# Kernel tuning notes

Measured on AMD Instinct MI355X. Metric: run time of the kernel, lower is better.

## Reference

```python
import jax, jax.numpy as jnp
import numpy as np

K = 27        # 3^3 kernel offsets for kernel_size=3, dimension=3
M = 50000     # kernel-map pairs per offset
N = 100000    # active voxels
C = 64        # channels
EPS = 1e-5


def setup_inputs() -> dict:
    key = jax.random.key(0)
    ks = jax.random.split(key, 5)
    scale = 1.0 / np.sqrt(K * C)
    return {
        "features": jax.random.normal(ks[0], (N, C), jnp.float32),
        "W1": jax.random.normal(ks[1], (K, C, C), jnp.float32) * scale,
        "gamma1": jnp.ones((C,), jnp.float32),
        "beta1": jnp.zeros((C,), jnp.float32),
        "W2": jax.random.normal(ks[2], (K, C, C), jnp.float32) * scale,
        "gamma2": jnp.ones((C,), jnp.float32),
        "beta2": jnp.zeros((C,), jnp.float32),
        "in_maps": jax.random.randint(ks[3], (K, M), 0, N, dtype=jnp.int32),
        "out_maps": jax.random.randint(ks[4], (K, M), 0, N, dtype=jnp.int32),
        "n": N,
    }


def sparse_conv(f, W, in_maps, out_maps, n):
    # gather-GEMM-scatter, the MinkowskiConvolution compute pattern
    gathered = f[in_maps]                              # [K, M, Cin]
    msgs = jnp.einsum('kmc,kcd->kmd', gathered, W)     # [K, M, Cout]
    cout = W.shape[-1]
    out = jnp.zeros((n, cout), f.dtype)
    return out.at[out_maps.reshape(-1)].add(msgs.reshape(-1, cout))


def batch_norm(x, gamma, beta):
    # BatchNorm1d over the [N, C] sparse feature matrix (training-mode batch stats)
    mu = x.mean(axis=0)
    var = x.var(axis=0)
    return (x - mu) * jax.lax.rsqrt(var + EPS) * gamma + beta


def reference(features, W1, gamma1, beta1, W2, gamma2, beta2, in_maps, out_maps, n):
    out = sparse_conv(features, W1, in_maps, out_maps, n)
    out = jax.nn.relu(batch_norm(out, gamma1, beta1))
    out = sparse_conv(out, W2, in_maps, out_maps, n)
    out = batch_norm(out, gamma2, beta2)
    # stride=1 and in_channels==out_channels -> downsample is None
    return jax.nn.relu(out + features)
```

## Files before the change

### kernel.cpp

```cpp
#include <hip/hip_runtime.h>

typedef __attribute__((ext_vector_type(8))) short bf16x8;
typedef __attribute__((ext_vector_type(4))) float f32x4;

#define KK 27
#define MM 50000
#define NV 100000
#define CC 64
#define EPSV 1e-5f
#define PPB 400

__device__ inline void split2(float x, unsigned short& h, unsigned short& l) {
    const unsigned u  = __float_as_uint(x);
    const unsigned hb = u & 0xFFFF0000u;
    h = (unsigned short)(hb >> 16);
    const float r = x - __uint_as_float(hb);
    const unsigned v = __float_as_uint(r);
    l = (unsigned short)((v + 0x7FFFu + ((v >> 16) & 1u)) >> 16);
}

__device__ inline unsigned short rne_bf16(float x) {
    const unsigned u = __float_as_uint(x);
    return (unsigned short)((u + 0x7FFFu + ((u >> 16) & 1u)) >> 16);
}

__global__ __launch_bounds__(256)
void split_planes(const float* __restrict__ x, unsigned short* __restrict__ P) {
    const int i = blockIdx.x * 256 + threadIdx.x;
    const int r = i >> 5, c2 = (i & 31) * 2;
    const float2 v = *(const float2*)(x + (size_t)r * CC + c2);
    unsigned short h0, l0, h1, l1;
    split2(v.x, h0, l0);
    split2(v.y, h1, l1);
    *(unsigned int*)(P + (size_t)r * 128 + c2)      = (unsigned)h0 | ((unsigned)h1 << 16);
    *(unsigned int*)(P + (size_t)r * 128 + 64 + c2) = (unsigned)l0 | ((unsigned)l1 << 16);
}

__global__ __launch_bounds__(256)
void csr_hist(const int* __restrict__ outm, int* __restrict__ cnt) {
    const int e = blockIdx.x * 256 + threadIdx.x;
    if (e < KK * MM) atomicAdd(&cnt[outm[e]], 1);
}

__global__ __launch_bounds__(1024)
void scan1(const int* __restrict__ cnt, int* __restrict__ off, int* __restrict__ bsum) {
    __shared__ int tmp[1024];
    const int t = threadIdx.x;
    const int i = blockIdx.x * 1024 + t;
    const int v = (i < NV) ? cnt[i] : 0;
    tmp[t] = v;
    __syncthreads();
    for (int d = 1; d < 1024; d <<= 1) {
        const int add = (t >= d) ? tmp[t - d] : 0;
        __syncthreads();
        tmp[t] += add;
        __syncthreads();
    }
    if (i < NV) off[i] = tmp[t] - v;
    if (t == 1023) bsum[blockIdx.x] = tmp[1023];
}

__global__ __launch_bounds__(128)
void scan2(int* __restrict__ bsum, int nb) {
    __shared__ int tmp[128];
    const int t = threadIdx.x;
    const int v = (t < nb) ? bsum[t] : 0;
    tmp[t] = v;
    __syncthreads();
    for (int d = 1; d < 128; d <<= 1) {
        const int add = (t >= d) ? tmp[t - d] : 0;
        __syncthreads();
        tmp[t] += add;
        __syncthreads();
    }
    if (t < nb) bsum[t] = tmp[t] - v;
}

__global__ __launch_bounds__(256)
void scan3(int* __restrict__ off, const int* __restrict__ bsum) {
    const int i = blockIdx.x * 256 + threadIdx.x;
    if (i < NV) off[i] += bsum[i >> 10];
    if (i == 0) off[NV] = KK * MM;
}

__global__ __launch_bounds__(256)
void csr_fill(const int* __restrict__ outm, const int* __restrict__ off,
              int* __restrict__ cur, int* __restrict__ dst) {
    const int e = blockIdx.x * 256 + threadIdx.x;
    if (e >= KK * MM) return;
    const int row = outm[e];
    const int pos = atomicAdd(&cur[row], 1);
    dst[e] = off[row] + pos;
}

#define MF(a, b, c) c = __builtin_amdgcn_mfma_f32_16x16x32_bf16(a, b, c, 0, 0, 0)

__global__ __launch_bounds__(256, 3)
void conv_gemm(const unsigned short* __restrict__ P, const float* __restrict__ W,
               const int* __restrict__ inm_all, const int* __restrict__ dst,
               unsigned short* __restrict__ msgs) {
    const int k   = blockIdx.y;
    const int L   = threadIdx.x & 63;
    const int wv  = threadIdx.x >> 6;
    const int g   = L >> 4;
    const int c16 = L & 15;

    __shared__ float lds[4352];

    {
        const float4* Wg  = (const float4*)(W + (size_t)k * CC * CC);
        float4*       Wl4 = (float4*)lds;
#pragma unroll
        for (int i = 0; i < 4; ++i)
            Wl4[threadIdx.x + 256 * i] = Wg[threadIdx.x + 256 * i];
    }
    __syncthreads();

    bf16x8 Wh[2][4], Wlo[2][4];
#pragma unroll
    for (int s = 0; s < 2; ++s)
#pragma unroll
        for (int t = 0; t < 4; ++t)
#pragma unroll
            for (int j = 0; j < 8; ++j) {
                const float w = lds[(g * 8 + j + 32 * s) * CC + 16 * t + c16];
                unsigned short h, lo;
                split2(w, h, lo);
                Wh[s][t][j]  = (short)h;
                Wlo[s][t][j] = (short)lo;
            }
    __syncthreads();

    float* ldsC = lds + wv * 1088;

    const int* inm = inm_all + (size_t)k * MM;
    const int pstart = blockIdx.x * PPB;
    const int pend   = min(MM, pstart + PPB);

    int base = pstart + wv * 16;
    if (base + 16 > pend) return;

    const unsigned short* rp = P + (size_t)inm[base + c16] * 128;
    bf16x8 ah0 = *(const bf16x8*)(rp +      g * 8);
    bf16x8 ah1 = *(const bf16x8*)(rp + 32 + g * 8);
    bf16x8 al0 = *(const bf16x8*)(rp + 64 + g * 8);
    bf16x8 al1 = *(const bf16x8*)(rp + 96 + g * 8);

    while (true) {
        const int  nbase = base + 64;
        const bool hasn  = (nbase + 16 <= pend);
        bf16x8 nh0, nh1, nl0, nl1;
        if (hasn) {
            const unsigned short* np = P + (size_t)inm[nbase + c16] * 128;
            nh0 = *(const bf16x8*)(np +      g * 8);
            nh1 = *(const bf16x8*)(np + 32 + g * 8);
            nl0 = *(const bf16x8*)(np + 64 + g * 8);
            nl1 = *(const bf16x8*)(np + 96 + g * 8);
        }

        f32x4 acc0 = {0.f, 0.f, 0.f, 0.f}, acc1 = acc0, acc2 = acc0, acc3 = acc0;
        MF(ah0, Wh[0][0], acc0); MF(ah0, Wh[0][1], acc1); MF(ah0, Wh[0][2], acc2); MF(ah0, Wh[0][3], acc3);
        MF(ah1, Wh[1][0], acc0); MF(ah1, Wh[1][1], acc1); MF(ah1, Wh[1][2], acc2); MF(ah1, Wh[1][3], acc3);
        MF(al0, Wh[0][0], acc0); MF(al0, Wh[0][1], acc1); MF(al0, Wh[0][2], acc2); MF(al0, Wh[0][3], acc3);
        MF(al1, Wh[1][0], acc0); MF(al1, Wh[1][1], acc1); MF(al1, Wh[1][2], acc2); MF(al1, Wh[1][3], acc3);
        MF(ah0, Wlo[0][0], acc0); MF(ah0, Wlo[0][1], acc1); MF(ah0, Wlo[0][2], acc2); MF(ah0, Wlo[0][3], acc3);
        MF(ah1, Wlo[1][0], acc0); MF(ah1, Wlo[1][1], acc1); MF(ah1, Wlo[1][2], acc2); MF(ah1, Wlo[1][3], acc3);

#pragma unroll
        for (int j = 0; j < 4; ++j) {
            ldsC[(g * 4 + j) * 68 +      c16] = acc0[j];
            ldsC[(g * 4 + j) * 68 + 16 + c16] = acc1[j];
            ldsC[(g * 4 + j) * 68 + 32 + c16] = acc2[j];
            ldsC[(g * 4 + j) * 68 + 48 + c16] = acc3[j];
        }
        const int e0 = k * MM + base;
#pragma unroll
        for (int r = 0; r < 16; ++r) {
            const int d = dst[e0 + r];
            msgs[(size_t)d * CC + L] = rne_bf16(ldsC[r * 68 + L]);
        }

        if (!hasn) break;
        base = nbase;
        ah0 = nh0; ah1 = nh1; al0 = nl0; al1 = nl1;
    }
}

__global__ __launch_bounds__(256)
void csr_reduce_stats(const unsigned short* __restrict__ msgs,
                      const int* __restrict__ off,
                      float* __restrict__ out, float* __restrict__ stats) {
    const int L   = threadIdx.x & 63;
    const int wv  = threadIdx.x >> 6;
    const int q   = L & 15;
    const int sub = L >> 4;

    float sum0 = 0.f, sum1 = 0.f, sum2 = 0.f, sum3 = 0.f;
    float ssq0 = 0.f, ssq1 = 0.f, ssq2 = 0.f, ssq3 = 0.f;

    for (int n = blockIdx.x * 4 + wv; n < NV; n += gridDim.x * 4) {
        const int s = off[n], e = off[n + 1];
        float a0 = 0.f, a1 = 0.f, a2 = 0.f, a3 = 0.f;
        for (int i = s + sub; i < e; i += 4) {
            const uint2 v = *(const uint2*)(msgs + (size_t)i * CC + q * 4);
            a0 += __uint_as_float(v.x << 16);
            a1 += __uint_as_float(v.x & 0xFFFF0000u);
            a2 += __uint_as_float(v.y << 16);
            a3 += __uint_as_float(v.y & 0xFFFF0000u);
        }
        a0 += __shfl_xor(a0, 16); a1 += __shfl_xor(a1, 16);
        a2 += __shfl_xor(a2, 16); a3 += __shfl_xor(a3, 16);
        a0 += __shfl_xor(a0, 32); a1 += __shfl_xor(a1, 32);
        a2 += __shfl_xor(a2, 32); a3 += __shfl_xor(a3, 32);
        if (sub == 0) {
            const float4 r = {a0, a1, a2, a3};
            *(float4*)(out + (size_t)n * CC + q * 4) = r;
            sum0 += a0; ssq0 = fmaf(a0, a0, ssq0);
            sum1 += a1; ssq1 = fmaf(a1, a1, ssq1);
            sum2 += a2; ssq2 = fmaf(a2, a2, ssq2);
            sum3 += a3; ssq3 = fmaf(a3, a3, ssq3);
        }
    }

    __shared__ float red[2][4][CC];
    if (sub == 0) {
        red[0][wv][q * 4 + 0] = sum0; red[1][wv][q * 4 + 0] = ssq0;
        red[0][wv][q * 4 + 1] = sum1; red[1][wv][q * 4 + 1] = ssq1;
        red[0][wv][q * 4 + 2] = sum2; red[1][wv][q * 4 + 2] = ssq2;
        red[0][wv][q * 4 + 3] = sum3; red[1][wv][q * 4 + 3] = ssq3;
    }
    __syncthreads();
    if (threadIdx.x < CC) {
        const int c = threadIdx.x;
        const float ts  = red[0][0][c] + red[0][1][c] + red[0][2][c] + red[0][3][c];
        const float tss = red[1][0][c] + red[1][1][c] + red[1][2][c] + red[1][3][c];
        atomicAdd(&stats[c], ts);
        atomicAdd(&stats[CC + c], tss);
    }
}

__global__ __launch_bounds__(256)
void bn_relu_split(const float* __restrict__ x, const float* __restrict__ stats,
                   const float* __restrict__ gamma, const float* __restrict__ beta,
                   unsigned short* __restrict__ P) {
    const int i = blockIdx.x * 256 + threadIdx.x;
    const int r = i >> 5, c2 = (i & 31) * 2;
    float sc[2], sh[2];
#pragma unroll
    for (int j = 0; j < 2; ++j) {
        const int   c    = c2 + j;
        const float mu   = stats[c] * (1.f / NV);
        const float var  = fmaf(-mu, mu, stats[CC + c] * (1.f / NV));
        const float istd = rsqrtf(var + EPSV);
        sc[j] = gamma[c] * istd;
        sh[j] = fmaf(-mu, sc[j], beta[c]);
    }
    const float2 v = *(const float2*)(x + (size_t)r * CC + c2);
    const float y0 = fmaxf(fmaf(v.x, sc[0], sh[0]), 0.f);
    const float y1 = fmaxf(fmaf(v.y, sc[1], sh[1]), 0.f);
    unsigned short h0, l0, h1, l1;
    split2(y0, h0, l0);
    split2(y1, h1, l1);
    *(unsigned int*)(P + (size_t)r * 128 + c2)      = (unsigned)h0 | ((unsigned)h1 << 16);
    *(unsigned int*)(P + (size_t)r * 128 + 64 + c2) = (unsigned)l0 | ((unsigned)l1 << 16);
}

__global__ __launch_bounds__(256)
void bn_res_relu(float* __restrict__ x, const float* __restrict__ feat,
                 const float* __restrict__ stats,
                 const float* __restrict__ gamma, const float* __restrict__ beta) {
    const int tid   = blockIdx.x * blockDim.x + threadIdx.x;
    const int total = NV * CC / 4;
    const int cbase = (tid * 4) & (CC - 1);
    float scale[4], shift[4];
#pragma unroll
    for (int j = 0; j < 4; ++j) {
        const int   c    = cbase + j;
        const float mu   = stats[c] * (1.f / NV);
        const float var  = fmaf(-mu, mu, stats[CC + c] * (1.f / NV));
        const float istd = rsqrtf(var + EPSV);
        scale[j] = gamma[c] * istd;
        shift[j] = fmaf(-mu, scale[j], beta[c]);
    }
    float4*       x4 = (float4*)x;
    const float4* f4 = (const float4*)feat;
    for (int i = tid; i < total; i += gridDim.x * blockDim.x) {
        float4 v = x4[i];
        const float4 fr = f4[i];
        v.x = fmaxf(fmaf(v.x, scale[0], shift[0]) + fr.x, 0.f);
        v.y = fmaxf(fmaf(v.y, scale[1], shift[1]) + fr.y, 0.f);
        v.z = fmaxf(fmaf(v.z, scale[2], shift[2]) + fr.z, 0.f);
        v.w = fmaxf(fmaf(v.w, scale[3], shift[3]) + fr.w, 0.f);
        x4[i] = v;
    }
}

extern "C" void kernel_launch(void* const* d_in, const int* in_sizes, int n_in,
                              void* d_out, int out_size, void* d_ws, size_t ws_size,
                              hipStream_t stream) {
    const float* features = (const float*)d_in[0];
    const float* W1       = (const float*)d_in[1];
    const float* gamma1   = (const float*)d_in[2];
    const float* beta1    = (const float*)d_in[3];
    const float* W2       = (const float*)d_in[4];
    const float* gamma2   = (const float*)d_in[5];
    const float* beta2    = (const float*)d_in[6];
    const int*   in_maps  = (const int*)d_in[7];
    const int*   out_maps = (const int*)d_in[8];

    float* out = (float*)d_out;

    unsigned short* P     = (unsigned short*)d_ws;
    float*          stats = (float*)(P + (size_t)NV * 128);
    int*            cnt   = (int*)(stats + 256);
    int*            cur   = cnt + NV;
    int*            off   = cur + NV;
    int*            dst   = off + NV + 8;
    int*            bsum  = dst + KK * MM;
    unsigned short* msgs  = (unsigned short*)(bsum + 256);

    dim3 cgrid(MM / PPB, KK);

    hipMemsetAsync(stats, 0, (256 + 2 * NV) * sizeof(int), stream);

    split_planes<<<12500, 256, 0, stream>>>(features, P);

    csr_hist<<<(KK * MM + 255) / 256, 256, 0, stream>>>(out_maps, cnt);
    const int nb = (NV + 1023) / 1024;
    scan1<<<nb, 1024, 0, stream>>>(cnt, off, bsum);
    scan2<<<1, 128, 0, stream>>>(bsum, nb);
    scan3<<<(NV + 255) / 256, 256, 0, stream>>>(off, bsum);
    csr_fill<<<(KK * MM + 255) / 256, 256, 0, stream>>>(out_maps, off, cur, dst);

    conv_gemm<<<cgrid, 256, 0, stream>>>(P, W1, in_maps, dst, msgs);
    csr_reduce_stats<<<2048, 256, 0, stream>>>(msgs, off, out, stats);
    bn_relu_split<<<12500, 256, 0, stream>>>(out, stats, gamma1, beta1, P);

    conv_gemm<<<cgrid, 256, 0, stream>>>(P, W2, in_maps, dst, msgs);
    csr_reduce_stats<<<2048, 256, 0, stream>>>(msgs, off, out, stats + 128);
    bn_res_relu<<<1024, 256, 0, stream>>>(out, features, stats + 128, gamma2, beta2);
}
```

Before: 599.6 us.

## Merge CSR build and reduce/BN stages into cooperative grid-sync kernels

Replaces the six CSR-building and plane-split launches with one cooperative kernel that uses grid.sync between phases, and folds each BN/ReLU (or residual) pass into the reduction kernel after a grid-wide sync on the stats. The block scan now handles four elements per thread with 256 threads. conv_gemm's launch bounds are raised from 3 to 6 blocks per SM, which tightens the register budget. The aim is to cut launch gaps and tail effects. The cost is grid-sync overhead and a fixed 1024-block grid, where the reduction previously used 2048 blocks.

```diff
diff --git a/kernel.cpp b/kernel.cpp
--- a/kernel.cpp
+++ b/kernel.cpp
@@ -1,4 +1,7 @@
 #include <hip/hip_runtime.h>
+#include <hip/hip_cooperative_groups.h>
+
+namespace cg = cooperative_groups;
 
 typedef __attribute__((ext_vector_type(8))) short bf16x8;
 typedef __attribute__((ext_vector_type(4))) float f32x4;
@@ -25,77 +28,86 @@
 }
 
 __global__ __launch_bounds__(256)
-void split_planes(const float* __restrict__ x, unsigned short* __restrict__ P) {
-    const int i = blockIdx.x * 256 + threadIdx.x;
-    const int r = i >> 5, c2 = (i & 31) * 2;
-    const float2 v = *(const float2*)(x + (size_t)r * CC + c2);
-    unsigned short h0, l0, h1, l1;
-    split2(v.x, h0, l0);
-    split2(v.y, h1, l1);
-    *(unsigned int*)(P + (size_t)r * 128 + c2)      = (unsigned)h0 | ((unsigned)h1 << 16);
-    *(unsigned int*)(P + (size_t)r * 128 + 64 + c2) = (unsigned)l0 | ((unsigned)l1 << 16);
-}
-
-__global__ __launch_bounds__(256)
-void csr_hist(const int* __restrict__ outm, int* __restrict__ cnt) {
-    const int e = blockIdx.x * 256 + threadIdx.x;
-    if (e < KK * MM) atomicAdd(&cnt[outm[e]], 1);
-}
-
-__global__ __launch_bounds__(1024)
-void scan1(const int* __restrict__ cnt, int* __restrict__ off, int* __restrict__ bsum) {
-    __shared__ int tmp[1024];
-    const int t = threadIdx.x;
-    const int i = blockIdx.x * 1024 + t;
-    const int v = (i < NV) ? cnt[i] : 0;
-    tmp[t] = v;
-    __syncthreads();
-    for (int d = 1; d < 1024; d <<= 1) {
-        const int add = (t >= d) ? tmp[t - d] : 0;
+void build_coop(const float* __restrict__ x, unsigned short* __restrict__ P,
+                const int* __restrict__ outm,
+                int* __restrict__ cnt, int* __restrict__ cur,
+                int* __restrict__ off, int* __restrict__ dst,
+                int* __restrict__ bsum) {
+    cg::grid_group grid = cg::this_grid();
+    const int tid = blockIdx.x * 256 + threadIdx.x;
+    const int nth = gridDim.x * 256;
+
+    for (int i = tid; i < NV * 32; i += nth) {
+        const int r = i >> 5, c2 = (i & 31) * 2;
+        const float2 v = *(const float2*)(x + (size_t)r * CC + c2);
+        unsigned short h0, l0, h1, l1;
+        split2(v.x, h0, l0);
+        split2(v.y, h1, l1);
+        *(unsigned int*)(P + (size_t)r * 128 + c2)      = (unsigned)h0 | ((unsigned)h1 << 16);
+        *(unsigned int*)(P + (size_t)r * 128 + 64 + c2) = (unsigned)l0 | ((unsigned)l1 << 16);
+    }
+    for (int e = tid; e < KK * MM; e += nth) atomicAdd(&cnt[outm[e]], 1);
+    grid.sync();
+
+    if (blockIdx.x < (NV + 1023) / 1024) {
+        const int t    = threadIdx.x;
+        const int base = blockIdx.x * 1024 + t * 4;
+        int v[4], ts = 0;
+#pragma unroll
+        for (int j = 0; j < 4; ++j) {
+            v[j] = (base + j < NV) ? cnt[base + j] : 0;
+            ts += v[j];
+        }
+        __shared__ int ps[256];
+        ps[t] = ts;
         __syncthreads();
-        tmp[t] += add;
+        for (int d = 1; d < 256; d <<= 1) {
+            const int a = (t >= d) ? ps[t - d] : 0;
+            __syncthreads();
+            ps[t] += a;
+            __syncthreads();
+        }
+        int run = ps[t] - ts;
+#pragma unroll
+        for (int j = 0; j < 4; ++j) {
+            if (base + j < NV) off[base + j] = run;
+            run += v[j];
+        }
+        if (t == 255) bsum[blockIdx.x] = ps[255];
+    }
+    grid.sync();
+
+    if (blockIdx.x == 0) {
+        const int nb = (NV + 1023) / 1024;
+        const int t  = threadIdx.x;
+        __shared__ int tmp[256];
+        const int v = (t < nb) ? bsum[t] : 0;
+        tmp[t] = v;
         __syncthreads();
-    }
-    if (i < NV) off[i] = tmp[t] - v;
-    if (t == 1023) bsum[blockIdx.x] = tmp[1023];
-}
-
-__global__ __launch_bounds__(128)
-void scan2(int* __restrict__ bsum, int nb) {
-    __shared__ int tmp[128];
-    const int t = threadIdx.x;
-    const int v = (t < nb) ? bsum[t] : 0;
-    tmp[t] = v;
-    __syncthreads();
-    for (int d = 1; d < 128; d <<= 1) {
-        const int add = (t >= d) ? tmp[t - d] : 0;
-        __syncthreads();
-        tmp[t] += add;
-        __syncthreads();
-    }
-    if (t < nb) bsum[t] = tmp[t] - v;
-}
-
-__global__ __launch_bounds__(256)
-void scan3(int* __restrict__ off, const int* __restrict__ bsum) {
-    const int i = blockIdx.x * 256 + threadIdx.x;
-    if (i < NV) off[i] += bsum[i >> 10];
-    if (i == 0) off[NV] = KK * MM;
-}
-
-__global__ __launch_bounds__(256)
-void csr_fill(const int* __restrict__ outm, const int* __restrict__ off,
-              int* __restrict__ cur, int* __restrict__ dst) {
-    const int e = blockIdx.x * 256 + threadIdx.x;
-    if (e >= KK * MM) return;
-    const int row = outm[e];
-    const int pos = atomicAdd(&cur[row], 1);
-    dst[e] = off[row] + pos;
+        for (int d = 1; d < 256; d <<= 1) {
+            const int a = (t >= d) ? tmp[t - d] : 0;
+            __syncthreads();
+            tmp[t] += a;
+            __syncthreads();
+        }
+        if (t < nb) bsum[t] = tmp[t] - v;
+    }
+    grid.sync();
+
+    for (int i = tid; i < NV; i += nth) off[i] += bsum[i >> 10];
+    if (tid == 0) off[NV] = KK * MM;
+    grid.sync();
+
+    for (int e = tid; e < KK * MM; e += nth) {
+        const int row = outm[e];
+        const int pos = atomicAdd(&cur[row], 1);
+        dst[e] = off[row] + pos;
+    }
 }
 
 #define MF(a, b, c) c = __builtin_amdgcn_mfma_f32_16x16x32_bf16(a, b, c, 0, 0, 0)
 
-__global__ __launch_bounds__(256, 3)
+__global__ __launch_bounds__(256, 6)
 void conv_gemm(const unsigned short* __restrict__ P, const float* __restrict__ W,
                const int* __restrict__ inm_all, const int* __restrict__ dst,
                unsigned short* __restrict__ msgs) {
@@ -186,10 +198,13 @@
     }
 }
 
+template <int RES>
 __global__ __launch_bounds__(256)
-void csr_reduce_stats(const unsigned short* __restrict__ msgs,
-                      const int* __restrict__ off,
-                      float* __restrict__ out, float* __restrict__ stats) {
+void reduce_coop(const unsigned short* __restrict__ msgs, const int* __restrict__ off,
+                 float* __restrict__ out, float* __restrict__ stats,
+                 const float* __restrict__ gamma, const float* __restrict__ beta,
+                 unsigned short* __restrict__ P, const float* __restrict__ feat) {
+    cg::grid_group grid = cg::this_grid();
     const int L   = threadIdx.x & 63;
     const int wv  = threadIdx.x >> 6;
     const int q   = L & 15;
@@ -232,66 +247,60 @@
     __syncthreads();
     if (threadIdx.x < CC) {
         const int c = threadIdx.x;
-        const float ts  = red[0][0][c] + red[0][1][c] + red[0][2][c] + red[0][3][c];
-        const float tss = red[1][0][c] + red[1][1][c] + red[1][2][c] + red[1][3][c];
-        atomicAdd(&stats[c], ts);
-        atomicAdd(&stats[CC + c], tss);
-    }
-}
-
-__global__ __launch_bounds__(256)
-void bn_relu_split(const float* __restrict__ x, const float* __restrict__ stats,
-                   const float* __restrict__ gamma, const float* __restrict__ beta,
-                   unsigned short* __restrict__ P) {
-    const int i = blockIdx.x * 256 + threadIdx.x;
-    const int r = i >> 5, c2 = (i & 31) * 2;
-    float sc[2], sh[2];
-#pragma unroll
-    for (int j = 0; j < 2; ++j) {
-        const int   c    = c2 + j;
-        const float mu   = stats[c] * (1.f / NV);
-        const float var  = fmaf(-mu, mu, stats[CC + c] * (1.f / NV));
-        const float istd = rsqrtf(var + EPSV);
-        sc[j] = gamma[c] * istd;
-        sh[j] = fmaf(-mu, sc[j], beta[c]);
-    }
-    const float2 v = *(const float2*)(x + (size_t)r * CC + c2);
-    const float y0 = fmaxf(fmaf(v.x, sc[0], sh[0]), 0.f);
-    const float y1 = fmaxf(fmaf(v.y, sc[1], sh[1]), 0.f);
-    unsigned short h0, l0, h1, l1;
-    split2(y0, h0, l0);
-    split2(y1, h1, l1);
-    *(unsigned int*)(P + (size_t)r * 128 + c2)      = (unsigned)h0 | ((unsigned)h1 << 16);
-    *(unsigned int*)(P + (size_t)r * 128 + 64 + c2) = (unsigned)l0 | ((unsigned)l1 << 16);
-}
-
-__global__ __launch_bounds__(256)
-void bn_res_relu(float* __restrict__ x, const float* __restrict__ feat,
-                 const float* __restrict__ stats,
-                 const float* __restrict__ gamma, const float* __restrict__ beta) {
-    const int tid   = blockIdx.x * blockDim.x + threadIdx.x;
-    const int total = NV * CC / 4;
-    const int cbase = (tid * 4) & (CC - 1);
-    float scale[4], shift[4];
-#pragma unroll
-    for (int j = 0; j < 4; ++j) {
-        const int   c    = cbase + j;
-        const float mu   = stats[c] * (1.f / NV);
-        const float var  = fmaf(-mu, mu, stats[CC + c] * (1.f / NV));
-        const float istd = rsqrtf(var + EPSV);
-        scale[j] = gamma[c] * istd;
-        shift[j] = fmaf(-mu, scale[j], beta[c]);
-    }
-    float4*       x4 = (float4*)x;
-    const float4* f4 = (const float4*)feat;
-    for (int i = tid; i < total; i += gridDim.x * blockDim.x) {
-        float4 v = x4[i];
-        const float4 fr = f4[i];
-        v.x = fmaxf(fmaf(v.x, scale[0], shift[0]) + fr.x, 0.f);
-        v.y = fmaxf(fmaf(v.y, scale[1], shift[1]) + fr.y, 0.f);
-        v.z = fmaxf(fmaf(v.z, scale[2], shift[2]) + fr.z, 0.f);
-        v.w = fmaxf(fmaf(v.w, scale[3], shift[3]) + fr.w, 0.f);
-        x4[i] = v;
+        atomicAdd(&stats[c],      red[0][0][c] + red[0][1][c] + red[0][2][c] + red[0][3][c]);
+        atomicAdd(&stats[CC + c], red[1][0][c] + red[1][1][c] + red[1][2][c] + red[1][3][c]);
+    }
+
+    grid.sync();
+
+    const int tid = blockIdx.x * 256 + threadIdx.x;
+    const int nth = gridDim.x * 256;
+    if (RES == 0) {
+        for (int i = tid; i < NV * 32; i += nth) {
+            const int r = i >> 5, c2 = (i & 31) * 2;
+            float sc[2], sh[2];
+#pragma unroll
+            for (int j = 0; j < 2; ++j) {
+                const int   c    = c2 + j;
+                const float mu   = stats[c] * (1.f / NV);
+                const float var  = fmaf(-mu, mu, stats[CC + c] * (1.f / NV));
+                const float istd = rsqrtf(var + EPSV);
+                sc[j] = gamma[c] * istd;
+                sh[j] = fmaf(-mu, sc[j], beta[c]);
+            }
+            const float2 v = *(const float2*)(out + (size_t)r * CC + c2);
+            const float y0 = fmaxf(fmaf(v.x, sc[0], sh[0]), 0.f);
+            const float y1 = fmaxf(fmaf(v.y, sc[1], sh[1]), 0.f);
+            unsigned short h0, l0, h1, l1;
+            split2(y0, h0, l0);
+            split2(y1, h1, l1);
+            *(unsigned int*)(P + (size_t)r * 128 + c2)      = (unsigned)h0 | ((unsigned)h1 << 16);
+            *(unsigned int*)(P + (size_t)r * 128 + 64 + c2) = (unsigned)l0 | ((unsigned)l1 << 16);
+        }
+    } else {
+        const int total = NV * CC / 4;
+        const int cbase = (tid * 4) & (CC - 1);
+        float scale[4], shift[4];
+#pragma unroll
+        for (int j = 0; j < 4; ++j) {
+            const int   c    = cbase + j;
+            const float mu   = stats[c] * (1.f / NV);
+            const float var  = fmaf(-mu, mu, stats[CC + c] * (1.f / NV));
+            const float istd = rsqrtf(var + EPSV);
+            scale[j] = gamma[c] * istd;
+            shift[j] = fmaf(-mu, scale[j], beta[c]);
+        }
+        float4*       x4 = (float4*)out;
+        const float4* f4 = (const float4*)feat;
+        for (int i = tid; i < total; i += nth) {
+            float4 v = x4[i];
+            const float4 fr = f4[i];
+            v.x = fmaxf(fmaf(v.x, scale[0], shift[0]) + fr.x, 0.f);
+            v.y = fmaxf(fmaf(v.y, scale[1], shift[1]) + fr.y, 0.f);
+            v.z = fmaxf(fmaf(v.z, scale[2], shift[2]) + fr.z, 0.f);
+            v.w = fmaxf(fmaf(v.w, scale[3], shift[3]) + fr.w, 0.f);
+            x4[i] = v;
+        }
     }
 }
 
@@ -323,20 +332,31 @@
 
     hipMemsetAsync(stats, 0, (256 + 2 * NV) * sizeof(int), stream);
 
-    split_planes<<<12500, 256, 0, stream>>>(features, P);
-
-    csr_hist<<<(KK * MM + 255) / 256, 256, 0, stream>>>(out_maps, cnt);
-    const int nb = (NV + 1023) / 1024;
-    scan1<<<nb, 1024, 0, stream>>>(cnt, off, bsum);
-    scan2<<<1, 128, 0, stream>>>(bsum, nb);
-    scan3<<<(NV + 255) / 256, 256, 0, stream>>>(off, bsum);
-    csr_fill<<<(KK * MM + 255) / 256, 256, 0, stream>>>(out_maps, off, cur, dst);
+    {
+        void* args[] = {(void*)&features, (void*)&P, (void*)&out_maps,
+                        (void*)&cnt, (void*)&cur, (void*)&off, (void*)&dst,
+                        (void*)&bsum};
+        hipLaunchCooperativeKernel((void*)build_coop, dim3(1024), dim3(256),
+                                   args, 0, stream);
+    }
 
     conv_gemm<<<cgrid, 256, 0, stream>>>(P, W1, in_maps, dst, msgs);
-    csr_reduce_stats<<<2048, 256, 0, stream>>>(msgs, off, out, stats);
-    bn_relu_split<<<12500, 256, 0, stream>>>(out, stats, gamma1, beta1, P);
+
+    {
+        float* st = stats;
+        void* args[] = {(void*)&msgs, (void*)&off, (void*)&out, (void*)&st,
+                        (void*)&gamma1, (void*)&beta1, (void*)&P, (void*)&features};
+        hipLaunchCooperativeKernel((void*)reduce_coop<0>, dim3(1024), dim3(256),
+                                   args, 0, stream);
+    }
 
     conv_gemm<<<cgrid, 256, 0, stream>>>(P, W2, in_maps, dst, msgs);
-    csr_reduce_stats<<<2048, 256, 0, stream>>>(msgs, off, out, stats + 128);
-    bn_res_relu<<<1024, 256, 0, stream>>>(out, features, stats + 128, gamma2, beta2);
-}
+
+    {
+        float* st = stats + 128;
+        void* args[] = {(void*)&msgs, (void*)&off, (void*)&out, (void*)&st,
+                        (void*)&gamma2, (void*)&beta2, (void*)&P, (void*)&features};
+        hipLaunchCooperativeKernel((void*)reduce_coop<1>, dim3(1024), dim3(256),
+                                   args, 0, stream);
+    }
+}
```

Result: slower. 1.807 ms (+201.4%).
